# Performance work log

Measured on AMD Instinct MI355X. Metric: run time of the kernel, lower is better.

## Reference

```python
import jax, jax.numpy as jnp
import numpy as np

N_NODES = 2000
GCN_OUT = 8
HID = 256
N_STEPS_OUT = 4


def setup_inputs() -> dict:
    key = jax.random.key(0)
    ks = jax.random.split(key, 16)
    B, S, N, E, F, H = 32, 24, N_NODES, 16000, GCN_OUT, HID
    I = F * N  # LSTM input size = gcn_out_features * num_nodes
    s = 0.05
    inp = {
        "x_sequences": jax.random.normal(ks[0], (B, S, N), jnp.float32),
        "edge_index": jax.random.randint(ks[1], (B, S, 2, E), 0, N, jnp.int32),
        "edge_distances": jax.random.uniform(ks[2], (B, S, E), jnp.float32),
        # CustomGCNLayer params (linear 1->F)
        "W_gcn": jax.random.normal(ks[3], (1, F), jnp.float32) * s,
        "b_gcn": jnp.zeros((F,), jnp.float32),
        # 2-layer LSTM (PyTorch layout: [4H, in], gate order i,f,g,o)
        "Wih0": jax.random.normal(ks[4], (4 * H, I), jnp.float32) * s,
        "Whh0": jax.random.normal(ks[5], (4 * H, H), jnp.float32) * s,
        "bih0": jnp.zeros((4 * H,), jnp.float32),
        "bhh0": jnp.zeros((4 * H,), jnp.float32),
        "Wih1": jax.random.normal(ks[6], (4 * H, H), jnp.float32) * s,
        "Whh1": jax.random.normal(ks[7], (4 * H, H), jnp.float32) * s,
        "bih1": jnp.zeros((4 * H,), jnp.float32),
        "bhh1": jnp.zeros((4 * H,), jnp.float32),
        # fc: hidden -> n_steps_out * num_nodes * num_node_features
        "fc_W": jax.random.normal(ks[8], (N_STEPS_OUT * N, H), jnp.float32) * s,
        "fc_b": jnp.zeros((N_STEPS_OUT * N,), jnp.float32),
    }
    return inp


def _lstm_layer(x, Wih, Whh, bih, bhh):
    # x: [B, S, in] -> hs: [B, S, H]
    B = x.shape[0]
    H = Whh.shape[1]
    b = bih + bhh

    def step(carry, xt):
        h, c = carry
        gates = xt @ Wih.T + h @ Whh.T + b  # [B, 4H]
        i, f, g, o = jnp.split(gates, 4, axis=-1)
        i = jax.nn.sigmoid(i)
        f = jax.nn.sigmoid(f)
        g = jnp.tanh(g)
        o = jax.nn.sigmoid(o)
        c = f * c + i * g
        h = o * jnp.tanh(c)
        return (h, c), h

    init = (jnp.zeros((B, H), x.dtype), jnp.zeros((B, H), x.dtype))
    _, hs = jax.lax.scan(step, init, x.transpose(1, 0, 2))  # time-major
    return hs.transpose(1, 0, 2)


def reference(x_sequences, edge_index, edge_distances, W_gcn, b_gcn,
              Wih0, Whh0, bih0, bhh0, Wih1, Whh1, bih1, bhh1, fc_W, fc_b):
    B, S, N = x_sequences.shape
    F = W_gcn.shape[1]
    # GCN layer (batched over all B*S graph snapshots):
    # h = x @ W + b ; out[i] = sum_{(j->i)} dist_e * h[j]
    h = x_sequences[..., None] * W_gcn[0] + b_gcn        # [B,S,N,F]
    src = edge_index[:, :, 0].reshape(B * S, -1)         # [BS,E]
    dst = edge_index[:, :, 1].reshape(B * S, -1)
    dist = edge_distances.reshape(B * S, -1)
    h2 = h.reshape(B * S, N, F)
    msgs = jnp.take_along_axis(h2, src[:, :, None], axis=1) * dist[..., None]  # [BS,E,F]
    agg = jax.vmap(lambda m, d: jax.ops.segment_sum(m, d, num_segments=N))(msgs, dst)
    gcn_seq = jnp.tanh(agg.reshape(B, S, N * F))         # [B,S,N*F]

    h1 = _lstm_layer(gcn_seq, Wih0, Whh0, bih0, bhh0)
    h2l = _lstm_layer(h1, Wih1, Whh1, bih1, bhh1)
    last = jnp.tanh(h2l)[:, -1, :]                       # [B,H]
    out = last @ fc_W.T + fc_b                           # [B, n_steps_out*N]
    n_steps_out = fc_b.shape[0] // N
    return out.reshape(B, n_steps_out, N)                # num_node_features=1 squeezed
```

## Files before the change

### kernel.cpp

```cpp
#include <hip/hip_runtime.h>

#define DEVINL __device__ __forceinline__

typedef __attribute__((ext_vector_type(8))) short bf16x8;
typedef __attribute__((ext_vector_type(4))) float f32x4;
typedef _Float16 half2_t __attribute__((ext_vector_type(2)));
typedef _Float16 f16x8 __attribute__((ext_vector_type(8)));

DEVINL unsigned short f2bf(float f) {
  unsigned int u = __float_as_uint(f);
  u += 0x7FFFu + ((u >> 16) & 1u);
  return (unsigned short)(u >> 16);
}
DEVINL unsigned short f2h(float f) {
  return __builtin_bit_cast(unsigned short, (_Float16)f);
}
DEVINL float sigmf(float x) { return 1.f / (1.f + __expf(-x)); }
DEVINL float tanh_fast(float x) { float e = __expf(2.f * x); return 1.f - 2.f / (e + 1.f); }

DEVINL float fdot2u(unsigned int h, unsigned int w, float acc) {
  return __builtin_amdgcn_fdot2(__builtin_bit_cast(half2_t, h),
                                __builtin_bit_cast(half2_t, w), acc, false);
}

DEVINL void gload_lds16(const void* g, void* l) {
  __builtin_amdgcn_global_load_lds(
      (const __attribute__((address_space(1))) void*)g,
      (__attribute__((address_space(3))) void*)l, 16, 0, 0);
}


__global__ __launch_bounds__(256) void conv_bf16(const float* __restrict__ in,
                                                 unsigned short* __restrict__ out) {
  int id = blockIdx.x * 256 + threadIdx.x;
  float4 v = *(const float4*)&in[(size_t)id * 4];
  unsigned int a = (unsigned int)f2bf(v.x) | ((unsigned int)f2bf(v.y) << 16);
  unsigned int b = (unsigned int)f2bf(v.z) | ((unsigned int)f2bf(v.w) << 16);
  *(uint2*)&out[(size_t)id * 4] = make_uint2(a, b);
}

__global__ __launch_bounds__(256) void conv_f16(const float* __restrict__ in,
                                                unsigned short* __restrict__ out) {
  int id = blockIdx.x * 256 + threadIdx.x;
  out[id] = f2h(in[id]);
}

__global__ __launch_bounds__(256) void pack_whh_g(const float* __restrict__ in,
                                                  uint2* __restrict__ out) {
  int id = blockIdx.x * 256 + threadIdx.x;
  int g = id >> 14;
  int rem = id & 16383;
  int u2 = rem >> 8;
  int c = rem & 255;
  int col = (c >> 6) * 256 + g * 64 + (c & 63);
  float4 v = *(const float4*)&in[col * 256 + u2 * 4];
  unsigned int p0 = (unsigned int)f2h(v.x) | ((unsigned int)f2h(v.y) << 16);
  unsigned int p1 = (unsigned int)f2h(v.z) | ((unsigned int)f2h(v.w) << 16);
  out[id] = make_uint2(p0, p1);
}

#define FXSCALE 1048576.f
#define FXINV   (1.f / 1048576.f)

__global__ __launch_bounds__(1024) void gcn_kernel(
    const float* __restrict__ x, const int* __restrict__ ei, const float* __restrict__ ed,
    const float* __restrict__ Wg, const float* __restrict__ bg,
    unsigned short* __restrict__ G) {
  __shared__ float xs[2000];
  __shared__ int Ai[2000];
  __shared__ int Di[2000];
  int bs = blockIdx.x;
  int tid = threadIdx.x;
  for (int i = tid; i < 2000; i += 1024) {
    xs[i] = x[(size_t)bs * 2000 + i];
    Ai[i] = 0; Di[i] = 0;
  }
  bool bgz = (bg[0] == 0.f) && (bg[1] == 0.f) && (bg[2] == 0.f) && (bg[3] == 0.f) &&
             (bg[4] == 0.f) && (bg[5] == 0.f) && (bg[6] == 0.f) && (bg[7] == 0.f);
  __syncthreads();
  const int* srcp = ei + (size_t)bs * 32000;
  const int* dstp = srcp + 16000;
  const float* dp = ed + (size_t)bs * 16000;
  if (bgz) {
#pragma unroll
    for (int ii = 0; ii < 3; ++ii) {
      int i = tid + ii * 1024;
      int4 s4 = ((const int4*)srcp)[i];
      int4 d4 = ((const int4*)dstp)[i];
      float4 w4 = ((const float4*)dp)[i];
      atomicAdd(&Ai[d4.x], __float2int_rn(w4.x * xs[s4.x] * FXSCALE));
      atomicAdd(&Ai[d4.y], __float2int_rn(w4.y * xs[s4.y] * FXSCALE));
      atomicAdd(&Ai[d4.z], __float2int_rn(w4.z * xs[s4.z] * FXSCALE));
      atomicAdd(&Ai[d4.w], __float2int_rn(w4.w * xs[s4.w] * FXSCALE));
    }
    if (tid < 928) {
      int i = tid + 3072;
      int4 s4 = ((const int4*)srcp)[i];
      int4 d4 = ((const int4*)dstp)[i];
      float4 w4 = ((const float4*)dp)[i];
      atomicAdd(&Ai[d4.x], __float2int_rn(w4.x * xs[s4.x] * FXSCALE));
      atomicAdd(&Ai[d4.y], __float2int_rn(w4.y * xs[s4.y] * FXSCALE));
      atomicAdd(&Ai[d4.z], __float2int_rn(w4.z * xs[s4.z] * FXSCALE));
      atomicAdd(&Ai[d4.w], __float2int_rn(w4.w * xs[s4.w] * FXSCALE));
    }
  } else {
    for (int i = tid; i < 4000; i += 1024) {
      int4 s4 = ((const int4*)srcp)[i];
      int4 d4 = ((const int4*)dstp)[i];
      float4 w4 = ((const float4*)dp)[i];
      atomicAdd(&Ai[d4.x], __float2int_rn(w4.x * xs[s4.x] * FXSCALE));
      atomicAdd(&Di[d4.x], __float2int_rn(w4.x * FXSCALE));
      atomicAdd(&Ai[d4.y], __float2int_rn(w4.y * xs[s4.y] * FXSCALE));
      atomicAdd(&Di[d4.y], __float2int_rn(w4.y * FXSCALE));
      atomicAdd(&Ai[d4.z], __float2int_rn(w4.z * xs[s4.z] * FXSCALE));
      atomicAdd(&Di[d4.z], __float2int_rn(w4.z * FXSCALE));
      atomicAdd(&Ai[d4.w], __float2int_rn(w4.w * xs[s4.w] * FXSCALE));
      atomicAdd(&Di[d4.w], __float2int_rn(w4.w * FXSCALE));
    }
  }
  __syncthreads();
  float wreg[8], breg[8];
#pragma unroll
  for (int f = 0; f < 8; ++f) { wreg[f] = Wg[f]; breg[f] = bg[f]; }
  for (int n = tid; n < 2000; n += 1024) {
    float a  = (float)Ai[n] * FXINV;
    float dd = (float)Di[n] * FXINV;
    unsigned int u[4];
#pragma unroll
    for (int p = 0; p < 4; ++p) {
      float v0 = tanh_fast(wreg[2 * p] * a + breg[2 * p] * dd);
      float v1 = tanh_fast(wreg[2 * p + 1] * a + breg[2 * p + 1] * dd);
      u[p] = (unsigned int)f2bf(v0) | ((unsigned int)f2bf(v1) << 16);
    }
    *(uint4*)&G[(size_t)bs * 16000 + n * 8] = make_uint4(u[0], u[1], u[2], u[3]);
  }
}

__global__ __launch_bounds__(256) void gemm_bt(
    const unsigned short* __restrict__ A, const unsigned short* __restrict__ B,
    float* __restrict__ Cp) {
  __shared__ __align__(16) unsigned short As[128 * 32];
  __shared__ __align__(16) unsigned short Bs[128 * 32];
  const int K = 16000;
  int nt = blockIdx.x;
  int mt = blockIdx.y;
  int ks = blockIdx.z;
  int m0 = mt * 128, n0 = nt * 128;
  int tid = threadIdx.x;
  int lane = tid & 63;
  int w = tid >> 6;
  int wm = (w >> 1) * 64, wn = (w & 1) * 64;
  int fr = lane & 15;
  int kg = lane >> 4;

  f32x4 acc[4][4] = {};
  const unsigned short* Ag = A + (size_t)m0 * K + ks * 1600;
  const unsigned short* Bg = B + (size_t)n0 * K + ks * 1600;

  for (int kk = 0; kk < 1600; kk += 32) {
#pragma unroll
    for (int q = 0; q < 2; ++q) {
      int c = q * 256 + tid;
      int row = c >> 2;
      int ko = (c & 3) * 8;
      int cb = q * 256 + (tid & ~63);
      gload_lds16(&Ag[(size_t)row * K + kk + ko], &As[cb * 8]);
      gload_lds16(&Bg[(size_t)row * K + kk + ko], &Bs[cb * 8]);
    }
    __syncthreads();
    bf16x8 aF[4], bF[4];
#pragma unroll
    for (int i = 0; i < 4; ++i)
      aF[i] = *(const bf16x8*)&As[(wm + i * 16 + fr) * 32 + kg * 8];
#pragma unroll
    for (int i = 0; i < 4; ++i)
      bF[i] = *(const bf16x8*)&Bs[(wn + i * 16 + fr) * 32 + kg * 8];
#pragma unroll
    for (int i = 0; i < 4; ++i)
#pragma unroll
      for (int j = 0; j < 4; ++j)
        acc[i][j] = __builtin_amdgcn_mfma_f32_16x16x32_bf16(aF[i], bF[j], acc[i][j], 0, 0, 0);
    __syncthreads();
  }
  float* Co = Cp + (size_t)ks * 768 * 1024;
  int mr = (lane >> 4) * 4;
#pragma unroll
  for (int i = 0; i < 4; ++i)
#pragma unroll
    for (int j = 0; j < 4; ++j) {
      int n = n0 + wn + j * 16 + fr;
#pragma unroll
      for (int r = 0; r < 4; ++r) {
        int m = m0 + wm + i * 16 + mr + r;
        Co[(size_t)m * 1024 + n] = acc[i][j][r];
      }
    }
}

__global__ __launch_bounds__(256) void reduce_z0(
    const float* __restrict__ Cp, const float* __restrict__ bih,
    const float* __restrict__ bhh, float* __restrict__ Z0) {
  int id = blockIdx.x * 256 + threadIdx.x;
  float s = bih[id & 1023] + bhh[id & 1023];
#pragma unroll
  for (int p = 0; p < 10; ++p) s += Cp[(size_t)p * 786432 + id];
  Z0[id] = s;
}

__global__ __launch_bounds__(1024) void lstm_sync2(
    const float* __restrict__ Z, const uint2* __restrict__ WPG,
    unsigned int* __restrict__ Hex, unsigned short* __restrict__ Hout,
    float* __restrict__ lastOut, int tagBase) {
  __shared__ __align__(16) uint2 Wl2[64 * 256];
  __shared__ float gparts[1024];
  __shared__ __align__(8) unsigned short h16[256];
  int bid = blockIdx.x;
  int b = bid >> 2, g = bid & 3;
  int tid = threadIdx.x;
  int lane = tid & 63;
  int c = tid & 255;
  int kh = __builtin_amdgcn_readfirstlane(tid >> 8);
  int q = c >> 6, r = c & 63;
  int col = q * 256 + g * 64 + r;

  const uint2* wsrc = WPG + (size_t)g * 16384;
  for (int i = tid; i < 16384; i += 1024) Wl2[i] = wsrc[i];
  if (tid < 128) ((unsigned int*)h16)[tid] = 0;
  __syncthreads();

  float cst = 0.f;
  const size_t b24 = (size_t)b * 24;

#pragma unroll 1
  for (int t = 0; t < 24; ++t) {
    uint2 hv = *(const uint2*)&((const unsigned int*)h16)[lane * 2];
    float acc = (kh == 0) ? Z[(b24 + t) * 1024 + col] : 0.f;
#pragma unroll
    for (int j = 0; j < 16; ++j) {
      const int u2i = kh * 16 + j;
      uint2 w2 = Wl2[u2i * 256 + c];
      unsigned int h0 = (unsigned int)__builtin_amdgcn_readlane((int)hv.x, u2i);
      unsigned int h1 = (unsigned int)__builtin_amdgcn_readlane((int)hv.y, u2i);
      acc = fdot2u(h0, w2.x, acc);
      acc = fdot2u(h1, w2.y, acc);
    }
    gparts[tid] = acc;
    __syncthreads();
    unsigned int* HexS = Hex + (t & 1) * 8192 + b * 256;
    if (tid < 64) {
      float i_ = gparts[tid]       + gparts[tid + 256]  + gparts[tid + 512]  + gparts[tid + 768];
      float f_ = gparts[tid + 64]  + gparts[tid + 320]  + gparts[tid + 576]  + gparts[tid + 832];
      float g_ = gparts[tid + 128] + gparts[tid + 384]  + gparts[tid + 640]  + gparts[tid + 896];
      float o_ = gparts[tid + 192] + gparts[tid + 448]  + gparts[tid + 704]  + gparts[tid + 960];
      float ig = sigmf(i_), fg = sigmf(f_);
      float gg = tanh_fast(g_), og = sigmf(o_);
      cst = fg * cst + ig * gg;
      float h = og * tanh_fast(cst);
      unsigned short hh = f2h(h);
      h16[g * 64 + tid] = hh;
      __hip_atomic_store(&HexS[g * 64 + tid],
                         (unsigned int)hh | ((unsigned int)(tagBase + t + 1) << 16),
                         __ATOMIC_RELAXED, __HIP_MEMORY_SCOPE_AGENT);
      if (Hout) Hout[(b24 + t) * 256 + g * 64 + tid] = hh;
      if (lastOut && t == 23) lastOut[b * 256 + g * 64 + tid] = tanh_fast(h);
    }
    if (t == 23) break;
    if (tid < 256 && (tid >> 6) != g) {
      const unsigned int tag = (unsigned int)(tagBase + t + 1);
      unsigned int v;
      do {
        v = __hip_atomic_load(&HexS[tid], __ATOMIC_RELAXED, __HIP_MEMORY_SCOPE_AGENT);
      } while ((v >> 16) != tag);
      h16[tid] = (unsigned short)(v & 0xFFFFu);
    }
    __syncthreads();
  }
}

__global__ __launch_bounds__(256) void gemm_z1_mfma(
    const unsigned short* __restrict__ A, const unsigned short* __restrict__ B,
    const float* __restrict__ bih, const float* __restrict__ bhh,
    float* __restrict__ Z1) {
  __shared__ __align__(16) unsigned short As[128 * 32];
  __shared__ __align__(16) unsigned short Bs[128 * 32];
  const int K = 256;
  int nt = blockIdx.x;
  int mt = blockIdx.y;
  int m0 = mt * 128, n0 = nt * 128;
  int tid = threadIdx.x;
  int lane = tid & 63;
  int w = tid >> 6;
  int wm = (w >> 1) * 64, wn = (w & 1) * 64;
  int fr = lane & 15;
  int kg = lane >> 4;

  f32x4 acc[4][4] = {};
  const unsigned short* Ag = A + (size_t)m0 * K;
  const unsigned short* Bg = B + (size_t)n0 * K;

  for (int kk = 0; kk < 256; kk += 32) {
#pragma unroll
    for (int q = 0; q < 2; ++q) {
      int c = q * 256 + tid;
      int row = c >> 2;
      int ko = (c & 3) * 8;
      int cb = q * 256 + (tid & ~63);
      gload_lds16(&Ag[(size_t)row * K + kk + ko], &As[cb * 8]);
      gload_lds16(&Bg[(size_t)row * K + kk + ko], &Bs[cb * 8]);
    }
    __syncthreads();
    f16x8 aF[4], bF[4];
#pragma unroll
    for (int i = 0; i < 4; ++i)
      aF[i] = *(const f16x8*)&As[(wm + i * 16 + fr) * 32 + kg * 8];
#pragma unroll
    for (int i = 0; i < 4; ++i)
      bF[i] = *(const f16x8*)&Bs[(wn + i * 16 + fr) * 32 + kg * 8];
#pragma unroll
    for (int i = 0; i < 4; ++i)
#pragma unroll
      for (int j = 0; j < 4; ++j)
        acc[i][j] = __builtin_amdgcn_mfma_f32_16x16x32_f16(aF[i], bF[j], acc[i][j], 0, 0, 0);
    __syncthreads();
  }
  int mr = (lane >> 4) * 4;
#pragma unroll
  for (int j = 0; j < 4; ++j) {
    int n = n0 + wn + j * 16 + fr;
    float bias = bih[n] + bhh[n];
#pragma unroll
    for (int i = 0; i < 4; ++i) {
#pragma unroll
      for (int r = 0; r < 4; ++r) {
        int m = m0 + wm + i * 16 + mr + r;
        Z1[(size_t)m * 1024 + n] = acc[i][j][r] + bias;
      }
    }
  }
}

__global__ __launch_bounds__(256) void fc_kernel(
    const float* __restrict__ last, const float* __restrict__ fcW,
    const float* __restrict__ fcb, float* __restrict__ out) {
  __shared__ float ls[8][256];
  int tid = threadIdx.x;
  int o = blockIdx.x * 256 + tid;
  int b0 = blockIdx.y * 8;
  for (int i = tid; i < 2048; i += 256)
    ls[i >> 8][i & 255] = last[(b0 + (i >> 8)) * 256 + (i & 255)];
  __syncthreads();
  if (o < 8000) {
    float acc[8] = {};
    for (int k = 0; k < 256; k += 4) {
      float4 wv = *(const float4*)&fcW[(size_t)o * 256 + k];
#pragma unroll
      for (int b = 0; b < 8; ++b)
        acc[b] += wv.x * ls[b][k] + wv.y * ls[b][k + 1] + wv.z * ls[b][k + 2] + wv.w * ls[b][k + 3];
    }
    float bias = fcb[o];
#pragma unroll
    for (int b = 0; b < 8; ++b) out[(size_t)(b0 + b) * 8000 + o] = acc[b] + bias;
  }
}

extern "C" void kernel_launch(void* const* d_in, const int* in_sizes, int n_in,
                              void* d_out, int out_size, void* d_ws, size_t ws_size,
                              hipStream_t stream) {
  const float* x    = (const float*)d_in[0];
  const int*   ei   = (const int*)d_in[1];
  const float* ed   = (const float*)d_in[2];
  const float* Wg   = (const float*)d_in[3];
  const float* bg   = (const float*)d_in[4];
  const float* Wih0 = (const float*)d_in[5];
  const float* Whh0 = (const float*)d_in[6];
  const float* bih0 = (const float*)d_in[7];
  const float* bhh0 = (const float*)d_in[8];
  const float* Wih1 = (const float*)d_in[9];
  const float* Whh1 = (const float*)d_in[10];
  const float* bih1 = (const float*)d_in[11];
  const float* bhh1 = (const float*)d_in[12];
  const float* fcW  = (const float*)d_in[13];
  const float* fcb  = (const float*)d_in[14];
  float* out = (float*)d_out;

  char* ws = (char*)d_ws;
  unsigned short* Gbf  = (unsigned short*)(ws);
  unsigned short* W0bf = (unsigned short*)(ws + 24576000);
  float* Zpart = (float*)(ws + 57344000);
  float* Z0    = (float*)(ws + 88801280);
  uint2* WPG0  = (uint2*)(ws + 91947008);
  uint2* WPG1  = (uint2*)(ws + 92471296);
  unsigned short* W1h = (unsigned short*)(ws + 92995584);
  unsigned short* H1  = (unsigned short*)(ws + 94044160);
  float* Z1    = (float*)(ws + 94830592);
  float* lastb = (float*)(ws + 97976320);
  unsigned int* Hex0 = (unsigned int*)(ws + 98009088);
  unsigned int* Hex1 = (unsigned int*)(ws + 98074624);

  hipMemsetAsync(Hex0, 0, 131072, stream);
  conv_bf16<<<16000, 256, 0, stream>>>(Wih0, W0bf);
  pack_whh_g<<<256, 256, 0, stream>>>(Whh0, WPG0);
  pack_whh_g<<<256, 256, 0, stream>>>(Whh1, WPG1);
  conv_f16<<<1024, 256, 0, stream>>>(Wih1, (unsigned short*)W1h);
  gcn_kernel<<<768, 1024, 0, stream>>>(x, ei, ed, Wg, bg, Gbf);
  gemm_bt<<<dim3(8, 6, 10), 256, 0, stream>>>(Gbf, W0bf, Zpart);
  reduce_z0<<<3072, 256, 0, stream>>>(Zpart, bih0, bhh0, Z0);
  lstm_sync2<<<128, 1024, 0, stream>>>(Z0, WPG0, Hex0, H1, nullptr, 0);
  gemm_z1_mfma<<<dim3(8, 6), 256, 0, stream>>>(H1, W1h, bih1, bhh1, Z1);
  lstm_sync2<<<128, 1024, 0, stream>>>(Z1, WPG1, Hex1, nullptr, lastb, 100);
  fc_kernel<<<dim3(32, 4), 256, 0, stream>>>(lastb, fcW, fcb, out);
}
```

Before: 251.9 us.

## Split GCN scatter into two-pass partial sums and double-buffer GEMM LDS staging

```diff
diff --git a/kernel.cpp b/kernel.cpp
--- a/kernel.cpp
+++ b/kernel.cpp
@@ -62,29 +62,27 @@
 #define FXSCALE 1048576.f
 #define FXINV   (1.f / 1048576.f)
 
-__global__ __launch_bounds__(1024) void gcn_kernel(
+__global__ __launch_bounds__(512) void gcn_pass1(
     const float* __restrict__ x, const int* __restrict__ ei, const float* __restrict__ ed,
-    const float* __restrict__ Wg, const float* __restrict__ bg,
-    unsigned short* __restrict__ G) {
+    const float* __restrict__ bg, float* __restrict__ Part) {
   __shared__ float xs[2000];
   __shared__ int Ai[2000];
   __shared__ int Di[2000];
-  int bs = blockIdx.x;
-  int tid = threadIdx.x;
-  for (int i = tid; i < 2000; i += 1024) {
+  int part = blockIdx.x & 1;
+  int bs = blockIdx.x >> 1;
+  int tid = threadIdx.x;
+  for (int i = tid; i < 2000; i += 512) {
     xs[i] = x[(size_t)bs * 2000 + i];
     Ai[i] = 0; Di[i] = 0;
   }
   bool bgz = (bg[0] == 0.f) && (bg[1] == 0.f) && (bg[2] == 0.f) && (bg[3] == 0.f) &&
              (bg[4] == 0.f) && (bg[5] == 0.f) && (bg[6] == 0.f) && (bg[7] == 0.f);
   __syncthreads();
-  const int* srcp = ei + (size_t)bs * 32000;
-  const int* dstp = srcp + 16000;
-  const float* dp = ed + (size_t)bs * 16000;
+  const int* srcp = ei + (size_t)bs * 32000 + part * 8000;
+  const int* dstp = ei + (size_t)bs * 32000 + 16000 + part * 8000;
+  const float* dp = ed + (size_t)bs * 16000 + part * 8000;
   if (bgz) {
-#pragma unroll
-    for (int ii = 0; ii < 3; ++ii) {
-      int i = tid + ii * 1024;
+    for (int i = tid; i < 2000; i += 512) {
       int4 s4 = ((const int4*)srcp)[i];
       int4 d4 = ((const int4*)dstp)[i];
       float4 w4 = ((const float4*)dp)[i];
@@ -93,18 +91,8 @@
       atomicAdd(&Ai[d4.z], __float2int_rn(w4.z * xs[s4.z] * FXSCALE));
       atomicAdd(&Ai[d4.w], __float2int_rn(w4.w * xs[s4.w] * FXSCALE));
     }
-    if (tid < 928) {
-      int i = tid + 3072;
-      int4 s4 = ((const int4*)srcp)[i];
-      int4 d4 = ((const int4*)dstp)[i];
-      float4 w4 = ((const float4*)dp)[i];
-      atomicAdd(&Ai[d4.x], __float2int_rn(w4.x * xs[s4.x] * FXSCALE));
-      atomicAdd(&Ai[d4.y], __float2int_rn(w4.y * xs[s4.y] * FXSCALE));
-      atomicAdd(&Ai[d4.z], __float2int_rn(w4.z * xs[s4.z] * FXSCALE));
-      atomicAdd(&Ai[d4.w], __float2int_rn(w4.w * xs[s4.w] * FXSCALE));
-    }
   } else {
-    for (int i = tid; i < 4000; i += 1024) {
+    for (int i = tid; i < 2000; i += 512) {
       int4 s4 = ((const int4*)srcp)[i];
       int4 d4 = ((const int4*)dstp)[i];
       float4 w4 = ((const float4*)dp)[i];
@@ -119,12 +107,27 @@
     }
   }
   __syncthreads();
+  float* P = Part + ((size_t)bs * 2 + part) * 4000;
+  for (int i = tid; i < 2000; i += 512) {
+    P[i] = (float)Ai[i] * FXINV;
+    if (!bgz) P[i + 2000] = (float)Di[i] * FXINV;
+  }
+}
+
+__global__ __launch_bounds__(256) void gcn_pass2(
+    const float* __restrict__ Part, const float* __restrict__ Wg,
+    const float* __restrict__ bg, unsigned short* __restrict__ G) {
+  int bs = blockIdx.x;
+  int tid = threadIdx.x;
+  bool bgz = (bg[0] == 0.f) && (bg[1] == 0.f) && (bg[2] == 0.f) && (bg[3] == 0.f) &&
+             (bg[4] == 0.f) && (bg[5] == 0.f) && (bg[6] == 0.f) && (bg[7] == 0.f);
+  const float* P = Part + (size_t)bs * 8000;
   float wreg[8], breg[8];
 #pragma unroll
   for (int f = 0; f < 8; ++f) { wreg[f] = Wg[f]; breg[f] = bg[f]; }
-  for (int n = tid; n < 2000; n += 1024) {
-    float a  = (float)Ai[n] * FXINV;
-    float dd = (float)Di[n] * FXINV;
+  for (int n = tid; n < 2000; n += 256) {
+    float a  = P[n] + P[n + 4000];
+    float dd = bgz ? 0.f : (P[n + 2000] + P[n + 6000]);
     unsigned int u[4];
 #pragma unroll
     for (int p = 0; p < 4; ++p) {
@@ -139,8 +142,8 @@
 __global__ __launch_bounds__(256) void gemm_bt(
     const unsigned short* __restrict__ A, const unsigned short* __restrict__ B,
     float* __restrict__ Cp) {
-  __shared__ __align__(16) unsigned short As[128 * 32];
-  __shared__ __align__(16) unsigned short Bs[128 * 32];
+  __shared__ __align__(16) unsigned short As[2][128 * 32];
+  __shared__ __align__(16) unsigned short Bs[2][128 * 32];
   const int K = 16000;
   int nt = blockIdx.x;
   int mt = blockIdx.y;
@@ -157,24 +160,30 @@
   const unsigned short* Ag = A + (size_t)m0 * K + ks * 1600;
   const unsigned short* Bg = B + (size_t)n0 * K + ks * 1600;
 
-  for (int kk = 0; kk < 1600; kk += 32) {
-#pragma unroll
-    for (int q = 0; q < 2; ++q) {
-      int c = q * 256 + tid;
-      int row = c >> 2;
-      int ko = (c & 3) * 8;
-      int cb = q * 256 + (tid & ~63);
-      gload_lds16(&Ag[(size_t)row * K + kk + ko], &As[cb * 8]);
-      gload_lds16(&Bg[(size_t)row * K + kk + ko], &Bs[cb * 8]);
-    }
-    __syncthreads();
+  int row0 = tid >> 2,            ko0 = (tid & 3) * 8,        cb0 = (tid & ~63);
+  int row1 = (256 + tid) >> 2,    ko1 = (tid & 3) * 8,        cb1 = 256 + (tid & ~63);
+
+#define STAGE_BT(buf, kk)                                                     \
+  do {                                                                        \
+    gload_lds16(&Ag[(size_t)row0 * K + (kk) + ko0], &As[buf][cb0 * 8]);       \
+    gload_lds16(&Bg[(size_t)row0 * K + (kk) + ko0], &Bs[buf][cb0 * 8]);       \
+    gload_lds16(&Ag[(size_t)row1 * K + (kk) + ko1], &As[buf][cb1 * 8]);       \
+    gload_lds16(&Bg[(size_t)row1 * K + (kk) + ko1], &Bs[buf][cb1 * 8]);       \
+  } while (0)
+
+  STAGE_BT(0, 0);
+  __syncthreads();
+#pragma unroll 1
+  for (int it = 0; it < 50; ++it) {
+    int cur = it & 1;
+    if (it < 49) STAGE_BT(cur ^ 1, (it + 1) * 32);
     bf16x8 aF[4], bF[4];
 #pragma unroll
     for (int i = 0; i < 4; ++i)
-      aF[i] = *(const bf16x8*)&As[(wm + i * 16 + fr) * 32 + kg * 8];
-#pragma unroll
-    for (int i = 0; i < 4; ++i)
-      bF[i] = *(const bf16x8*)&Bs[(wn + i * 16 + fr) * 32 + kg * 8];
+      aF[i] = *(const bf16x8*)&As[cur][(wm + i * 16 + fr) * 32 + kg * 8];
+#pragma unroll
+    for (int i = 0; i < 4; ++i)
+      bF[i] = *(const bf16x8*)&Bs[cur][(wn + i * 16 + fr) * 32 + kg * 8];
 #pragma unroll
     for (int i = 0; i < 4; ++i)
 #pragma unroll
@@ -182,6 +191,7 @@
         acc[i][j] = __builtin_amdgcn_mfma_f32_16x16x32_bf16(aF[i], bF[j], acc[i][j], 0, 0, 0);
     __syncthreads();
   }
+#undef STAGE_BT
   float* Co = Cp + (size_t)ks * 768 * 1024;
   int mr = (lane >> 4) * 4;
 #pragma unroll
@@ -402,7 +412,8 @@
   pack_whh_g<<<256, 256, 0, stream>>>(Whh0, WPG0);
   pack_whh_g<<<256, 256, 0, stream>>>(Whh1, WPG1);
   conv_f16<<<1024, 256, 0, stream>>>(Wih1, (unsigned short*)W1h);
-  gcn_kernel<<<768, 1024, 0, stream>>>(x, ei, ed, Wg, bg, Gbf);
+  gcn_pass1<<<1536, 512, 0, stream>>>(x, ei, ed, bg, Zpart);
+  gcn_pass2<<<768, 256, 0, stream>>>(Zpart, Wg, bg, Gbf);
   gemm_bt<<<dim3(8, 6, 10), 256, 0, stream>>>(Gbf, W0bf, Zpart);
   reduce_z0<<<3072, 256, 0, stream>>>(Zpart, bih0, bhh0, Z0);
   lstm_sync2<<<128, 1024, 0, stream>>>(Z0, WPG0, Hex0, H1, nullptr, 0);
```

After: 263.2 us. +4.5%, slower.
